# Kernel tuning notes

Measured on AMD Instinct MI355X. Metric: run time of the kernel, lower is better.

The kernel has to match this reference:

```python
import jax, jax.numpy as jnp
import numpy as np

N_GROUPS = 32
N_HEADS = 8
EPS = 1e-5


def group_norm(x, w, b):
    # x: [B, C, T]; GroupNorm32 computes in fp32 then casts back
    B, C, T = x.shape
    xf = x.astype(jnp.float32).reshape(B, N_GROUPS, (C // N_GROUPS) * T)
    mean = xf.mean(axis=-1, keepdims=True)
    var = xf.var(axis=-1, keepdims=True)
    xn = ((xf - mean) * jax.lax.rsqrt(var + EPS)).reshape(B, C, T)
    return (xn * w[None, :, None] + b[None, :, None]).astype(x.dtype)


def attention_block(x, norm_w, norm_b, qkv_w, qkv_b, proj_w, proj_b):
    B, C = x.shape[0], x.shape[1]
    spatial = x.shape[2:]
    xr = x.reshape(B, C, -1)  # [B, C, T]
    T = xr.shape[-1]
    h = group_norm(xr, norm_w, norm_b)
    # 1x1 Conv1d == per-position matmul: [B, 3C, T]
    qkv = jnp.einsum('oc,bct->bot', qkv_w, h) + qkv_b[None, :, None]
    ch = C // N_HEADS  # per-head channels
    q, k, v = jnp.split(qkv, 3, axis=1)
    q = q.reshape(B * N_HEADS, ch, T)
    k = k.reshape(B * N_HEADS, ch, T)
    v = v.reshape(B * N_HEADS, ch, T)
    scale = 1.0 / np.sqrt(ch)
    w = jnp.einsum('bct,bcs->bts', q * scale, k)  # [B*H, T, T]
    w = jax.nn.softmax(w.astype(jnp.float32), axis=-1).astype(w.dtype)
    a = jnp.einsum('bts,bcs->bct', w, v).reshape(B, C, T)
    a = jnp.einsum('oc,bct->bot', proj_w, a) + proj_b[None, :, None]
    return (xr + a).reshape(B, C, *spatial)


def setup_inputs() -> dict:
    key = jax.random.key(0)
    ks = jax.random.split(key, 6)
    B, C, H, W = 16, 512, 32, 32
    return {
        'x': jax.random.normal(ks[0], (B, C, H, W), jnp.float32),
        'norm_w': jnp.ones((C,), jnp.float32),
        'norm_b': jnp.zeros((C,), jnp.float32),
        'qkv_w': jax.random.normal(ks[1], (3 * C, C), jnp.float32) * (1.0 / np.sqrt(C)),
        'qkv_b': jax.random.normal(ks[2], (3 * C,), jnp.float32) * 0.02,
        'proj_w': jax.random.normal(ks[3], (C, C), jnp.float32) * (1.0 / np.sqrt(C)),
        'proj_b': jax.random.normal(ks[4], (C,), jnp.float32) * 0.02,
    }


def reference(x, norm_w, norm_b, qkv_w, qkv_b, proj_w, proj_b):
    return attention_block(x, norm_w, norm_b, qkv_w, qkv_b, proj_w, proj_b)
```

## Files before the change

### kernel.cpp

```cpp
#include <hip/hip_runtime.h>
#include <hip/hip_bf16.h>

#define B_ 16
#define C_ 512
#define T_ 1024
#define G_ 32
#define CPG 16
#define NH 8
#define CH 64
#define EPS 1e-5f

typedef __bf16 bf16x8 __attribute__((ext_vector_type(8)));
typedef __bf16 bf16x4 __attribute__((ext_vector_type(4)));
typedef float f32x4 __attribute__((ext_vector_type(4)));
typedef float f32x16 __attribute__((ext_vector_type(16)));
typedef int i32x4 __attribute__((ext_vector_type(4)));

__device__ __forceinline__ void gload16(const __bf16* g, const __bf16* l) {
    __builtin_amdgcn_global_load_lds(
        (const __attribute__((address_space(1))) unsigned int*)(unsigned long long)(uintptr_t)g,
        (__attribute__((address_space(3))) unsigned int*)(unsigned int)(uintptr_t)l,
        16, 0, 0);
}

__global__ __launch_bounds__(256) void prep_kernel(const float* __restrict__ x,
                                                   const float* __restrict__ w,
                                                   const float* __restrict__ bvec,
                                                   __bf16* __restrict__ h_t,
                                                   const float* __restrict__ qw,
                                                   const float* __restrict__ pw,
                                                   __bf16* __restrict__ wqb,
                                                   __bf16* __restrict__ wpb) {
    const int blk = blockIdx.x;
    if (blk >= 512) {
        int idx = ((blk - 512) * 256 + threadIdx.x) * 8;
        const float* src;
        __bf16* dst;
        if (idx < 1536 * 512) { src = qw + idx; dst = wqb + idx; }
        else { src = pw + (idx - 1536 * 512); dst = wpb + (idx - 1536 * 512); }
        float4 a = *(const float4*)src, b = *(const float4*)(src + 4);
        bf16x8 t;
        t[0] = (__bf16)a.x; t[1] = (__bf16)a.y; t[2] = (__bf16)a.z; t[3] = (__bf16)a.w;
        t[4] = (__bf16)b.x; t[5] = (__bf16)b.y; t[6] = (__bf16)b.z; t[7] = (__bf16)b.w;
        *(bf16x8*)dst = t;
        return;
    }
    const int bb = blk >> 5;
    const int g  = blk & 31;
    const size_t base = ((size_t)bb * C_ + (size_t)g * CPG) * T_;
    const float4* xp = (const float4*)(x + base);
    float4 vals[16];
    float s = 0.f, sq = 0.f;
#pragma unroll
    for (int i = 0; i < 16; ++i) {
        float4 v = xp[threadIdx.x + i * 256];
        vals[i] = v;
        s  += v.x + v.y + v.z + v.w;
        sq += v.x * v.x + v.y * v.y + v.z * v.z + v.w * v.w;
    }
#pragma unroll
    for (int off = 32; off > 0; off >>= 1) {
        s  += __shfl_down(s, off);
        sq += __shfl_down(sq, off);
    }
    __shared__ float red[2][4];
    const int lane = threadIdx.x & 63, wid = threadIdx.x >> 6;
    if (lane == 0) { red[0][wid] = s; red[1][wid] = sq; }
    __syncthreads();
    s  = red[0][0] + red[0][1] + red[0][2] + red[0][3];
    sq = red[1][0] + red[1][1] + red[1][2] + red[1][3];
    const float mean = s * (1.f / 16384.f);
    const float var  = sq * (1.f / 16384.f) - mean * mean;
    const float rstd = rsqrtf(var + EPS);
    float scv[16], shv[16];
#pragma unroll
    for (int i = 0; i < 16; ++i) {
        scv[i] = w[g * CPG + i] * rstd;
        shv[i] = bvec[g * CPG + i] - mean * scv[i];
    }
    __bf16* hb = h_t + ((size_t)bb * T_ + 4 * threadIdx.x) * C_ + g * CPG;
#pragma unroll
    for (int j = 0; j < 4; ++j) {
        bf16x8 t0, t1;
#pragma unroll
        for (int i = 0; i < 8; ++i) {
            float f0 = ((const float*)&vals[i])[j];
            float f1 = ((const float*)&vals[i + 8])[j];
            t0[i] = (__bf16)(f0 * scv[i] + shv[i]);
            t1[i] = (__bf16)(f1 * scv[i + 8] + shv[i + 8]);
        }
        *(bf16x8*)(hb + (size_t)j * C_) = t0;
        *(bf16x8*)(hb + (size_t)j * C_ + 8) = t1;
    }
}

template<int MODE>
__global__ __launch_bounds__(256) void gemm_mfma(const __bf16* __restrict__ Wb,
                                                 const float* __restrict__ bias,
                                                 const __bf16* __restrict__ Bin,
                                                 const float* __restrict__ xres,
                                                 __bf16* __restrict__ qt,
                                                 __bf16* __restrict__ kt,
                                                 __bf16* __restrict__ vb,
                                                 float* __restrict__ outp) {
    __shared__ __align__(16) __bf16 smem[18432];
    __bf16* As = smem;
    __bf16* Bt = smem + 8192;
    const int tid = threadIdx.x, lane = tid & 63, wv = tid >> 6;
    const int wr = wv >> 1, wc = wv & 1, frow = lane & 15, fgrp = lane >> 4;

    const int lin = blockIdx.x;
    int bz, o0, t0;
    if (MODE == 0) {
        const int work = (lin & 7) * 192 + (lin >> 3);
        const int yq = work % 12;
        const int rem = work / 12;
        bz = rem >> 3; o0 = yq << 7; t0 = (rem & 7) << 7;
    } else {
        const int work = (lin & 7) * 64 + (lin >> 3);
        const int yq = work & 3;
        const int rem = work >> 2;
        bz = rem >> 3; o0 = yq << 7; t0 = (rem & 7) << 7;
    }
    const int lrow = lane >> 3, lblk = (lane & 7) ^ (lrow & 7);

    const __bf16* gA = Wb + (size_t)(o0 + wv * 32 + lrow) * 512 + lblk * 8;
    const __bf16* gB = Bin + ((size_t)bz * T_ + t0 + wv * 32 + lrow) * 512 + lblk * 8;
    __bf16* lA = As + wv * 32 * 64;
    __bf16* lB = Bt + wv * 32 * 64;
    const int sb0 = (fgrp ^ (frow & 7)) * 8;
    const int sb1 = ((4 + fgrp) ^ (frow & 7)) * 8;

    f32x4 acc[4][4] = {};
    for (int k0 = 0; k0 < 512; k0 += 64) {
#pragma unroll
        for (int j = 0; j < 4; ++j) {
            gload16(gA + j * 4096 + k0, lA + j * 512);
            gload16(gB + j * 4096 + k0, lB + j * 512);
        }
        __syncthreads();
        bf16x8 af[4][2], bfr[4][2];
#pragma unroll
        for (int m = 0; m < 4; ++m) {
            const __bf16* r = As + (wr * 64 + m * 16 + frow) * 64;
            af[m][0] = *(const bf16x8*)(r + sb0);
            af[m][1] = *(const bf16x8*)(r + sb1);
        }
#pragma unroll
        for (int n = 0; n < 4; ++n) {
            const __bf16* r = Bt + (wc * 64 + n * 16 + frow) * 64;
            bfr[n][0] = *(const bf16x8*)(r + sb0);
            bfr[n][1] = *(const bf16x8*)(r + sb1);
        }
#pragma unroll
        for (int kk = 0; kk < 2; ++kk)
#pragma unroll
            for (int m = 0; m < 4; ++m)
#pragma unroll
                for (int n = 0; n < 4; ++n)
                    acc[m][n] = __builtin_amdgcn_mfma_f32_16x16x32_bf16(af[m][kk], bfr[n][kk], acc[m][n], 0, 0, 0);
        __syncthreads();
    }

    float bias_v[4][4];
#pragma unroll
    for (int m = 0; m < 4; ++m)
#pragma unroll
        for (int r = 0; r < 4; ++r)
            bias_v[m][r] = bias[o0 + wr * 64 + m * 16 + fgrp * 4 + r];

    __bf16* e = smem + wv * 4608;
    if (MODE == 0 && o0 < 1024) {
        const float qsc = (o0 < 512) ? 0.18033688f : 1.0f;
#pragma unroll
        for (int m = 0; m < 4; ++m)
#pragma unroll
            for (int n = 0; n < 4; ++n) {
                bf16x4 v;
#pragma unroll
                for (int r = 0; r < 4; ++r) v[r] = (__bf16)((acc[m][n][r] + bias_v[m][r]) * qsc);
                *(bf16x4*)&e[(n * 16 + frow) * 72 + m * 16 + fgrp * 4] = v;
            }
        __syncthreads();
        __bf16* dst = (o0 < 512) ? qt : kt;
        const int ob = o0 & 511;
#pragma unroll
        for (int p = 0; p < 8; ++p) {
            int row = p * 8 + (lane >> 3), c8 = (lane & 7) * 8;
            *(bf16x8*)(dst + ((size_t)bz * T_ + t0 + wc * 64 + row) * 512 + ob + wr * 64 + c8) =
                *(const bf16x8*)&e[row * 72 + c8];
        }
    } else {
#pragma unroll
        for (int m = 0; m < 4; ++m)
#pragma unroll
            for (int n = 0; n < 4; ++n)
#pragma unroll
                for (int r = 0; r < 4; ++r)
                    e[(m * 16 + fgrp * 4 + r) * 72 + n * 16 + frow] =
                        (__bf16)(acc[m][n][r] + bias_v[m][r]);
        __syncthreads();
        if (MODE == 0) {
            const int ob = o0 - 1024;
#pragma unroll
            for (int p = 0; p < 8; ++p) {
                int row = p * 8 + (lane >> 3), c8 = (lane & 7) * 8;
                *(bf16x8*)(vb + ((size_t)bz * C_ + ob + wr * 64 + row) * T_ + t0 + wc * 64 + c8) =
                    *(const bf16x8*)&e[row * 72 + c8];
            }
        } else {
#pragma unroll
            for (int p = 0; p < 8; ++p) {
                int row = p * 8 + (lane >> 3), c8 = (lane & 7) * 8;
                int o = o0 + wr * 64 + row;
                size_t base = ((size_t)bz * C_ + o) * T_ + t0 + wc * 64 + c8;
                bf16x8 v = *(const bf16x8*)&e[row * 72 + c8];
                float4 x0 = *(const float4*)(xres + base);
                float4 x1 = *(const float4*)(xres + base + 4);
                float4 r0, r1;
                r0.x = x0.x + (float)v[0]; r0.y = x0.y + (float)v[1];
                r0.z = x0.z + (float)v[2]; r0.w = x0.w + (float)v[3];
                r1.x = x1.x + (float)v[4]; r1.y = x1.y + (float)v[5];
                r1.z = x1.z + (float)v[6]; r1.w = x1.w + (float)v[7];
                *(float4*)(outp + base) = r0;
                *(float4*)(outp + base + 4) = r1;
            }
        }
    }
}

__global__ __launch_bounds__(256, 2) void attn32_kernel(const __bf16* __restrict__ qt,
                                                        const __bf16* __restrict__ kt,
                                                        const __bf16* __restrict__ vbuf,
                                                        __bf16* __restrict__ aout) {
    __shared__ __align__(16) __bf16 smem[18432];
    const int tid = threadIdx.x, lane = tid & 63, wv = tid >> 6;
    const int ln = lane & 31, hi = lane >> 5;
    const int lin = blockIdx.x;
    const int work = (lin & 7) * 64 + (lin >> 3);
    const int head = work >> 2;
    const int bb = head >> 3, hh = head & 7;
    const int tq0 = (work & 3) << 8;

    const __bf16* qbase = qt + (size_t)bb * T_ * 512 + hh * CH;
    const __bf16* kbase = kt + (size_t)bb * T_ * 512 + hh * CH;
    const __bf16* vbase = vbuf + ((size_t)bb * C_ + hh * CH) * T_;

    bf16x8 qf[2][4];
#pragma unroll
    for (int sub = 0; sub < 2; ++sub) {
        const __bf16* qr = qbase + (size_t)(tq0 + wv * 64 + sub * 32 + ln) * 512 + hi * 8;
#pragma unroll
        for (int st = 0; st < 4; ++st) qf[sub][st] = *(const bf16x8*)(qr + st * 16);
    }

    const int r8 = lane >> 3, cbs = (lane & 7) ^ (lane >> 3);
    const int rx = ln & 7;

    f32x16 o00 = {}, o01 = {}, o10 = {}, o11 = {};
    float l0 = 0.f, l1 = 0.f;

#pragma unroll
    for (int c = 0; c < 2; ++c) {
        int ch = wv * 2 + c;
        gload16(kbase + (size_t)(ch * 8 + r8) * 512 + cbs * 8, smem + ch * 512);
        gload16(vbase + (size_t)(ch * 8 + r8) * T_ + cbs * 8, smem + 4096 + ch * 512);
    }
    __syncthreads();

#pragma unroll 2
    for (int it = 0; it < 16; ++it) {
        const int cur = it & 1;
        if (it < 15) {
            const int s0n = (it + 1) << 6;
            __bf16* base = smem + (cur ^ 1) * 8192;
#pragma unroll
            for (int c = 0; c < 2; ++c) {
                int ch = wv * 2 + c;
                gload16(kbase + (size_t)(s0n + ch * 8 + r8) * 512 + cbs * 8, base + ch * 512);
                gload16(vbase + (size_t)(ch * 8 + r8) * T_ + s0n + cbs * 8, base + 4096 + ch * 512);
            }
        }
        const __bf16* Kb = smem + cur * 8192;
        const __bf16* Vb = Kb + 4096;

        f32x16 sa00 = {}, sa01 = {}, sa10 = {}, sa11 = {};
        {
            __builtin_amdgcn_s_setprio(1);
#pragma unroll
            for (int st = 0; st < 4; ++st) {
                const int cb = ((hi + 2 * st) ^ rx) << 3;
                bf16x8 k0 = *(const bf16x8*)(Kb + (size_t)ln * 64 + cb);
                bf16x8 k1 = *(const bf16x8*)(Kb + (size_t)(32 + ln) * 64 + cb);
                sa00 = __builtin_amdgcn_mfma_f32_32x32x16_bf16(k0, qf[0][st], sa00, 0, 0, 0);
                sa01 = __builtin_amdgcn_mfma_f32_32x32x16_bf16(k1, qf[0][st], sa01, 0, 0, 0);
                sa10 = __builtin_amdgcn_mfma_f32_32x32x16_bf16(k0, qf[1][st], sa10, 0, 0, 0);
                sa11 = __builtin_amdgcn_mfma_f32_32x32x16_bf16(k1, qf[1][st], sa11, 0, 0, 0);
            }
            __builtin_amdgcn_s_setprio(0);
        }

        float pa = 0.f, pb = 0.f, pc = 0.f, pd = 0.f;
#pragma unroll
        for (int i = 0; i < 16; ++i) { sa00[i] = __builtin_amdgcn_exp2f(sa00[i]); pa += sa00[i]; }
#pragma unroll
        for (int i = 0; i < 16; ++i) { sa01[i] = __builtin_amdgcn_exp2f(sa01[i]); pb += sa01[i]; }
#pragma unroll
        for (int i = 0; i < 16; ++i) { sa10[i] = __builtin_amdgcn_exp2f(sa10[i]); pc += sa10[i]; }
#pragma unroll
        for (int i = 0; i < 16; ++i) { sa11[i] = __builtin_amdgcn_exp2f(sa11[i]); pd += sa11[i]; }
        l0 += pa + pb;
        l1 += pc + pd;

        bf16x8 pfA[4], pfB[4];
#pragma unroll
        for (int sub = 0; sub < 2; ++sub) {
            const f32x16& s_lo = sub ? sa10 : sa00;
            const f32x16& s_hi = sub ? sa11 : sa01;
            unsigned Wd0[8], Wd1[8];
#pragma unroll
            for (int q = 0; q < 8; ++q) {
                unsigned a0 = (unsigned)__builtin_bit_cast(unsigned short, (__bf16)s_lo[2 * q]);
                unsigned a1 = (unsigned)__builtin_bit_cast(unsigned short, (__bf16)s_lo[2 * q + 1]);
                Wd0[q] = a0 | (a1 << 16);
                unsigned b0 = (unsigned)__builtin_bit_cast(unsigned short, (__bf16)s_hi[2 * q]);
                unsigned b1 = (unsigned)__builtin_bit_cast(unsigned short, (__bf16)s_hi[2 * q + 1]);
                Wd1[q] = b0 | (b1 << 16);
            }
            bf16x8* pf = sub ? pfB : pfA;
#pragma unroll
            for (int st = 0; st < 4; ++st) {
                const unsigned* W = (st >> 1) ? Wd1 : Wd0;
                const int hf = (st & 1) * 4;
                auto r02 = __builtin_amdgcn_permlane32_swap((int)W[hf + 0], (int)W[hf + 2], false, false);
                auto r13 = __builtin_amdgcn_permlane32_swap((int)W[hf + 1], (int)W[hf + 3], false, false);
                i32x4 pk;
                pk[0] = r02[0]; pk[1] = r13[0]; pk[2] = r02[1]; pk[3] = r13[1];
                pf[st] = __builtin_bit_cast(bf16x8, pk);
            }
        }

        {
            __builtin_amdgcn_s_setprio(1);
#pragma unroll
            for (int st = 0; st < 4; ++st) {
                const int cb = ((hi + 2 * st) ^ rx) << 3;
                bf16x8 v0 = *(const bf16x8*)(Vb + (size_t)ln * 64 + cb);
                bf16x8 v1 = *(const bf16x8*)(Vb + (size_t)(32 + ln) * 64 + cb);
                o00 = __builtin_amdgcn_mfma_f32_32x32x16_bf16(v0, pfA[st], o00, 0, 0, 0);
                o01 = __builtin_amdgcn_mfma_f32_32x32x16_bf16(v1, pfA[st], o01, 0, 0, 0);
                o10 = __builtin_amdgcn_mfma_f32_32x32x16_bf16(v0, pfB[st], o10, 0, 0, 0);
                o11 = __builtin_amdgcn_mfma_f32_32x32x16_bf16(v1, pfB[st], o11, 0, 0, 0);
            }
            __builtin_amdgcn_s_setprio(0);
        }
        __syncthreads();
    }

    l0 += __shfl_xor(l0, 32);
    l1 += __shfl_xor(l1, 32);
    const float rl0 = 1.f / l0, rl1 = 1.f / l1;
    __bf16* e = smem;
#pragma unroll
    for (int sub = 0; sub < 2; ++sub) {
        const float rl = sub ? rl1 : rl0;
        const int row = wv * 64 + sub * 32 + ln;
#pragma unroll
        for (int ct = 0; ct < 2; ++ct) {
            const f32x16& oc = sub ? (ct ? o11 : o10) : (ct ? o01 : o00);
#pragma unroll
            for (int q = 0; q < 8; ++q) {
                int c0 = ct * 32 + 2 * (q & 1) + 8 * (q >> 1) + 4 * hi;
                unsigned u0 = (unsigned)__builtin_bit_cast(unsigned short, (__bf16)(oc[2 * q] * rl));
                unsigned u1 = (unsigned)__builtin_bit_cast(unsigned short, (__bf16)(oc[2 * q + 1] * rl));
                *(unsigned*)&e[(size_t)row * 72 + c0] = u0 | (u1 << 16);
            }
        }
    }
    __syncthreads();
    {
        const int r = tid;
        __bf16* dst = aout + ((size_t)bb * T_ + tq0 + r) * 512 + hh * CH;
        const __bf16* er = e + (size_t)r * 72;
#pragma unroll
        for (int k = 0; k < 8; ++k)
            *(bf16x8*)(dst + k * 8) = *(const bf16x8*)(er + k * 8);
    }
}

extern "C" void kernel_launch(void* const* d_in, const int* in_sizes, int n_in,
                              void* d_out, int out_size, void* d_ws, size_t ws_size,
                              hipStream_t stream) {
    const float* x      = (const float*)d_in[0];
    const float* norm_w = (const float*)d_in[1];
    const float* norm_b = (const float*)d_in[2];
    const float* qkv_w  = (const float*)d_in[3];
    const float* qkv_b  = (const float*)d_in[4];
    const float* proj_w = (const float*)d_in[5];
    const float* proj_b = (const float*)d_in[6];
    float* out = (float*)d_out;

    __bf16* h_t = (__bf16*)d_ws;
    __bf16* wqb = h_t + (size_t)8388608;
    __bf16* wpb = wqb + 786432;
    __bf16* qt  = wpb + 262144;
    __bf16* kt  = qt + (size_t)8388608;
    __bf16* vb  = kt + (size_t)8388608;
    __bf16* at  = vb + (size_t)8388608;

    prep_kernel<<<1024, 256, 0, stream>>>(x, norm_w, norm_b, h_t, qkv_w, proj_w, wqb, wpb);
    gemm_mfma<0><<<dim3(1536), 256, 0, stream>>>(wqb, qkv_b, h_t, nullptr, qt, kt, vb, nullptr);
    attn32_kernel<<<dim3(512), 256, 0, stream>>>(qt, kt, vb, at);
    gemm_mfma<1><<<dim3(512), 256, 0, stream>>>(wpb, proj_b, at, x, nullptr, nullptr, nullptr, out);
}
```

Before: 109.6 us.

## Software-pipeline attention loop: overlap next QK with current softmax and PV

```diff
diff --git a/kernel.cpp b/kernel.cpp
--- a/kernel.cpp
+++ b/kernel.cpp
@@ -229,11 +229,11 @@
     }
 }
 
-__global__ __launch_bounds__(256, 2) void attn32_kernel(const __bf16* __restrict__ qt,
-                                                        const __bf16* __restrict__ kt,
-                                                        const __bf16* __restrict__ vbuf,
-                                                        __bf16* __restrict__ aout) {
-    __shared__ __align__(16) __bf16 smem[18432];
+__global__ __launch_bounds__(256) void attn32_kernel(const __bf16* __restrict__ qt,
+                                                     const __bf16* __restrict__ kt,
+                                                     const __bf16* __restrict__ vbuf,
+                                                     __bf16* __restrict__ aout) {
+    __shared__ __align__(16) __bf16 smem[24576];
     const int tid = threadIdx.x, lane = tid & 63, wv = tid >> 6;
     const int ln = lane & 31, hi = lane >> 5;
     const int lin = blockIdx.x;
@@ -260,63 +260,48 @@
     f32x16 o00 = {}, o01 = {}, o10 = {}, o11 = {};
     float l0 = 0.f, l1 = 0.f;
 
-#pragma unroll
-    for (int c = 0; c < 2; ++c) {
-        int ch = wv * 2 + c;
-        gload16(kbase + (size_t)(ch * 8 + r8) * 512 + cbs * 8, smem + ch * 512);
-        gload16(vbase + (size_t)(ch * 8 + r8) * T_ + cbs * 8, smem + 4096 + ch * 512);
-    }
-    __syncthreads();
-
-#pragma unroll 2
-    for (int it = 0; it < 16; ++it) {
-        const int cur = it & 1;
-        if (it < 15) {
-            const int s0n = (it + 1) << 6;
-            __bf16* base = smem + (cur ^ 1) * 8192;
-#pragma unroll
-            for (int c = 0; c < 2; ++c) {
-                int ch = wv * 2 + c;
-                gload16(kbase + (size_t)(s0n + ch * 8 + r8) * 512 + cbs * 8, base + ch * 512);
-                gload16(vbase + (size_t)(ch * 8 + r8) * T_ + s0n + cbs * 8, base + 4096 + ch * 512);
-            }
-        }
-        const __bf16* Kb = smem + cur * 8192;
-        const __bf16* Vb = Kb + 4096;
-
-        f32x16 sa00 = {}, sa01 = {}, sa10 = {}, sa11 = {};
-        {
-            __builtin_amdgcn_s_setprio(1);
-#pragma unroll
-            for (int st = 0; st < 4; ++st) {
-                const int cb = ((hi + 2 * st) ^ rx) << 3;
-                bf16x8 k0 = *(const bf16x8*)(Kb + (size_t)ln * 64 + cb);
-                bf16x8 k1 = *(const bf16x8*)(Kb + (size_t)(32 + ln) * 64 + cb);
-                sa00 = __builtin_amdgcn_mfma_f32_32x32x16_bf16(k0, qf[0][st], sa00, 0, 0, 0);
-                sa01 = __builtin_amdgcn_mfma_f32_32x32x16_bf16(k1, qf[0][st], sa01, 0, 0, 0);
-                sa10 = __builtin_amdgcn_mfma_f32_32x32x16_bf16(k0, qf[1][st], sa10, 0, 0, 0);
-                sa11 = __builtin_amdgcn_mfma_f32_32x32x16_bf16(k1, qf[1][st], sa11, 0, 0, 0);
-            }
-            __builtin_amdgcn_s_setprio(0);
-        }
-
+    auto STAGE = [&](int s0n, int bidx) {
+        __bf16* base = smem + bidx * 8192;
+#pragma unroll
+        for (int c = 0; c < 2; ++c) {
+            int ch = wv * 2 + c;
+            gload16(kbase + (size_t)(s0n + ch * 8 + r8) * 512 + cbs * 8, base + ch * 512);
+            gload16(vbase + (size_t)(ch * 8 + r8) * T_ + s0n + cbs * 8, base + 4096 + ch * 512);
+        }
+    };
+    auto QK = [&](int bidx, f32x16& s00, f32x16& s01, f32x16& s10, f32x16& s11) {
+        const __bf16* Kb = smem + bidx * 8192;
+        s00 = (f32x16){}; s01 = (f32x16){}; s10 = (f32x16){}; s11 = (f32x16){};
+        __builtin_amdgcn_s_setprio(1);
+#pragma unroll
+        for (int st = 0; st < 4; ++st) {
+            const int cb = ((hi + 2 * st) ^ rx) << 3;
+            bf16x8 k0 = *(const bf16x8*)(Kb + (size_t)ln * 64 + cb);
+            bf16x8 k1 = *(const bf16x8*)(Kb + (size_t)(32 + ln) * 64 + cb);
+            s00 = __builtin_amdgcn_mfma_f32_32x32x16_bf16(k0, qf[0][st], s00, 0, 0, 0);
+            s01 = __builtin_amdgcn_mfma_f32_32x32x16_bf16(k1, qf[0][st], s01, 0, 0, 0);
+            s10 = __builtin_amdgcn_mfma_f32_32x32x16_bf16(k0, qf[1][st], s10, 0, 0, 0);
+            s11 = __builtin_amdgcn_mfma_f32_32x32x16_bf16(k1, qf[1][st], s11, 0, 0, 0);
+        }
+        __builtin_amdgcn_s_setprio(0);
+    };
+    auto SMPV = [&](int bidx, f32x16& s00, f32x16& s01, f32x16& s10, f32x16& s11) {
         float pa = 0.f, pb = 0.f, pc = 0.f, pd = 0.f;
 #pragma unroll
-        for (int i = 0; i < 16; ++i) { sa00[i] = __builtin_amdgcn_exp2f(sa00[i]); pa += sa00[i]; }
-#pragma unroll
-        for (int i = 0; i < 16; ++i) { sa01[i] = __builtin_amdgcn_exp2f(sa01[i]); pb += sa01[i]; }
-#pragma unroll
-        for (int i = 0; i < 16; ++i) { sa10[i] = __builtin_amdgcn_exp2f(sa10[i]); pc += sa10[i]; }
-#pragma unroll
-        for (int i = 0; i < 16; ++i) { sa11[i] = __builtin_amdgcn_exp2f(sa11[i]); pd += sa11[i]; }
+        for (int i = 0; i < 16; ++i) { s00[i] = __builtin_amdgcn_exp2f(s00[i]); pa += s00[i]; }
+#pragma unroll
+        for (int i = 0; i < 16; ++i) { s01[i] = __builtin_amdgcn_exp2f(s01[i]); pb += s01[i]; }
+#pragma unroll
+        for (int i = 0; i < 16; ++i) { s10[i] = __builtin_amdgcn_exp2f(s10[i]); pc += s10[i]; }
+#pragma unroll
+        for (int i = 0; i < 16; ++i) { s11[i] = __builtin_amdgcn_exp2f(s11[i]); pd += s11[i]; }
         l0 += pa + pb;
         l1 += pc + pd;
-
         bf16x8 pfA[4], pfB[4];
 #pragma unroll
         for (int sub = 0; sub < 2; ++sub) {
-            const f32x16& s_lo = sub ? sa10 : sa00;
-            const f32x16& s_hi = sub ? sa11 : sa01;
+            const f32x16& s_lo = sub ? s10 : s00;
+            const f32x16& s_hi = sub ? s11 : s01;
             unsigned Wd0[8], Wd1[8];
 #pragma unroll
             for (int q = 0; q < 8; ++q) {
@@ -339,22 +324,39 @@
                 pf[st] = __builtin_bit_cast(bf16x8, pk);
             }
         }
-
-        {
-            __builtin_amdgcn_s_setprio(1);
-#pragma unroll
-            for (int st = 0; st < 4; ++st) {
-                const int cb = ((hi + 2 * st) ^ rx) << 3;
-                bf16x8 v0 = *(const bf16x8*)(Vb + (size_t)ln * 64 + cb);
-                bf16x8 v1 = *(const bf16x8*)(Vb + (size_t)(32 + ln) * 64 + cb);
-                o00 = __builtin_amdgcn_mfma_f32_32x32x16_bf16(v0, pfA[st], o00, 0, 0, 0);
-                o01 = __builtin_amdgcn_mfma_f32_32x32x16_bf16(v1, pfA[st], o01, 0, 0, 0);
-                o10 = __builtin_amdgcn_mfma_f32_32x32x16_bf16(v0, pfB[st], o10, 0, 0, 0);
-                o11 = __builtin_amdgcn_mfma_f32_32x32x16_bf16(v1, pfB[st], o11, 0, 0, 0);
-            }
-            __builtin_amdgcn_s_setprio(0);
-        }
-        __syncthreads();
+        const __bf16* Vb = smem + bidx * 8192 + 4096;
+        __builtin_amdgcn_s_setprio(1);
+#pragma unroll
+        for (int st = 0; st < 4; ++st) {
+            const int cb = ((hi + 2 * st) ^ rx) << 3;
+            bf16x8 v0 = *(const bf16x8*)(Vb + (size_t)ln * 64 + cb);
+            bf16x8 v1 = *(const bf16x8*)(Vb + (size_t)(32 + ln) * 64 + cb);
+            o00 = __builtin_amdgcn_mfma_f32_32x32x16_bf16(v0, pfA[st], o00, 0, 0, 0);
+            o01 = __builtin_amdgcn_mfma_f32_32x32x16_bf16(v1, pfA[st], o01, 0, 0, 0);
+            o10 = __builtin_amdgcn_mfma_f32_32x32x16_bf16(v0, pfB[st], o10, 0, 0, 0);
+            o11 = __builtin_amdgcn_mfma_f32_32x32x16_bf16(v1, pfB[st], o11, 0, 0, 0);
+        }
+        __builtin_amdgcn_s_setprio(0);
+    };
+
+    f32x16 saA00, saA01, saA10, saA11, saB00, saB01, saB10, saB11;
+    STAGE(0, 0);
+    STAGE(64, 1);
+    __syncthreads();
+    QK(0, saA00, saA01, saA10, saA11);
+
+    int ia = 0, ib = 1, ic = 2;
+    for (int i = 0; i < 16; i += 2) {
+        if (i + 2 < 16) STAGE((i + 2) << 6, ic);
+        if (i + 1 < 16) QK(ib, saB00, saB01, saB10, saB11);
+        SMPV(ia, saA00, saA01, saA10, saA11);
+        __syncthreads();
+        int tmp = ia; ia = ib; ib = ic; ic = tmp;
+        if (i + 3 < 16) STAGE((i + 3) << 6, ic);
+        if (i + 2 < 16) QK(ib, saA00, saA01, saA10, saA11);
+        SMPV(ia, saB00, saB01, saB10, saB11);
+        __syncthreads();
+        tmp = ia; ia = ib; ib = ic; ic = tmp;
     }
 
     l0 += __shfl_xor(l0, 32);
```

After: 121.0 us. +10.4%, slower.
